# Optimization experiments

Hardware: AMD Instinct MI355X
Metric: run time of the kernel (lower is better)

## Reference

```python
import jax, jax.numpy as jnp
import numpy as np

MAX_DIST = 3          # census patch radius -> 7x7 neighborhood
PATCH = 2 * MAX_DIST + 1


def _warp(img, flow):
    """Bilinear warp (Resample2d): sample img at (x + u, y + v). Coords clamped to border."""
    B, C, H, W = img.shape
    gy, gx = jnp.meshgrid(jnp.arange(H, dtype=img.dtype), jnp.arange(W, dtype=img.dtype), indexing='ij')
    x = gx[None] + flow[:, 0]           # [B,H,W]
    y = gy[None] + flow[:, 1]
    x0 = jnp.floor(x); y0 = jnp.floor(y)
    wx = x - x0; wy = y - y0            # bilinear weights
    x0i = jnp.clip(x0, 0, W - 1).astype(jnp.int32)
    x1i = jnp.clip(x0 + 1.0, 0, W - 1).astype(jnp.int32)
    y0i = jnp.clip(y0, 0, H - 1).astype(jnp.int32)
    y1i = jnp.clip(y0 + 1.0, 0, H - 1).astype(jnp.int32)

    def gather(im_b, yi, xi):           # im_b [C,H,W], yi/xi [H,W] -> [C,H,W]
        return im_b[:, yi, xi]
    g = jax.vmap(gather)
    Ia = g(img, y0i, x0i); Ib = g(img, y0i, x1i)
    Ic = g(img, y1i, x0i); Id = g(img, y1i, x1i)
    wx = wx[:, None]; wy = wy[:, None]  # [B,1,H,W]
    return Ia * (1 - wx) * (1 - wy) + Ib * wx * (1 - wy) + Ic * (1 - wx) * wy + Id * wx * wy


def _census_transform(image):
    """Ternary census transform: grayscale, extract 7x7 patches, normalized center differences."""
    gray = (0.299 * image[:, 0:1] + 0.587 * image[:, 1:2] + 0.114 * image[:, 2:3]) * 255.0
    w = jnp.eye(PATCH * PATCH, dtype=image.dtype).reshape(PATCH * PATCH, 1, PATCH, PATCH)
    patches = jax.lax.conv_general_dilated(
        gray, w, window_strides=(1, 1), padding=[(MAX_DIST, MAX_DIST)] * 2,
        dimension_numbers=('NCHW', 'OIHW', 'NCHW'))   # [B,49,H,W]
    t = patches - gray
    return t / jnp.sqrt(0.81 + t * t)


def _border_mask(B, H, W, dtype):
    m = jnp.zeros((H, W), dtype).at[MAX_DIST:H - MAX_DIST, MAX_DIST:W - MAX_DIST].set(1.0)
    return jnp.broadcast_to(m[None, None], (B, 1, H, W))


def _charbonnier(x, mask, alpha=0.45, eps=0.001):
    err = (x * x + eps * eps) ** alpha * mask
    return jnp.sum(err) / x.size


def _census_loss(im1, im2_warped, mask):
    t1 = _census_transform(im1)
    t2 = _census_transform(im2_warped)
    d = (t1 - t2) ** 2
    dist = jnp.sum(d / (0.1 + d), axis=1, keepdims=True)   # soft Hamming distance [B,1,H,W]
    B, _, H, W = dist.shape
    return _charbonnier(dist, mask * _border_mask(B, H, W, dist.dtype))


def setup_inputs() -> dict:
    key = jax.random.key(0)
    ks = jax.random.split(key, 6)
    B, H, W = 4, 320, 768
    return {
        'former': jax.random.uniform(ks[0], (B, 3, H, W), jnp.float32),
        'latter': jax.random.uniform(ks[1], (B, 3, H, W), jnp.float32),
        'disp_est_scale': jax.random.normal(ks[2], (B, 2, H, W), jnp.float32) * 3.0,
        'disp_est_scale_2': jax.random.normal(ks[3], (B, 2, H, W), jnp.float32) * 3.0,
        'fw_mask': jax.random.uniform(ks[4], (B, 1, H, W), jnp.float32),
        'bw_mask': jax.random.uniform(ks[5], (B, 1, H, W), jnp.float32),
    }


def reference(former, latter, disp_est_scale, disp_est_scale_2, fw_mask, bw_mask):
    left_est = _warp(latter, disp_est_scale)
    image_loss = _census_loss(former, left_est, fw_mask)
    right_est = _warp(former, disp_est_scale_2)
    image_loss_2 = _census_loss(latter, right_est, bw_mask)
    return (image_loss, image_loss_2)
```

## Files before the change

kernel.cpp:

```cpp
#include <hip/hip_runtime.h>

#define BB 4
#define H 320
#define W 768
#define P (H*W)
#define NPIX (BB*P)

#define TX 32
#define TY 8
#define TW (TX+6)
#define TH (TY+6)
#define HALO (TW*TH)
#define NBX (W/TX)
#define NBY (H/TY)
#define NBLK (NBX*NBY*BB)

typedef float f4 __attribute__((ext_vector_type(4)));

__global__ void gray_kernel(const float* __restrict__ former,
                            const float* __restrict__ latter,
                            float* __restrict__ gf, float* __restrict__ gl) {
    int idx = blockIdx.x * blockDim.x + threadIdx.x;
    if (idx >= NPIX) return;
    int b = idx / P;
    int r = idx - b * P;
    const float* f = former + (size_t)b * 3 * P + r;
    const float* l = latter + (size_t)b * 3 * P + r;
    gf[idx] = (0.299f * f[0] + 0.587f * f[P] + 0.114f * f[2 * P]) * 255.f;
    gl[idx] = (0.299f * l[0] + 0.587f * l[P] + 0.114f * l[2 * P]) * 255.f;
}

__device__ __forceinline__ float bilinear(const float* __restrict__ img, float fx, float fy) {
    float x0 = floorf(fx), y0 = floorf(fy);
    float wx = fx - x0, wy = fy - y0;
    float x0c = fminf(fmaxf(x0,       0.f), (float)(W - 1));
    float x1c = fminf(fmaxf(x0 + 1.f, 0.f), (float)(W - 1));
    float y0c = fminf(fmaxf(y0,       0.f), (float)(H - 1));
    float y1c = fminf(fmaxf(y0 + 1.f, 0.f), (float)(H - 1));
    int x0i = (int)x0c, x1i = (int)x1c, y0i = (int)y0c, y1i = (int)y1c;
    float Ia = img[y0i * W + x0i], Ib = img[y0i * W + x1i];
    float Ic = img[y1i * W + x0i], Id = img[y1i * W + x1i];
    float omx = 1.f - wx, omy = 1.f - wy;
    return Ia * omx * omy + Ib * wx * omy + Ic * omx * wy + Id * wx * wy;
}

__global__ __launch_bounds__(256, 5)
void fused_kernel(const float* __restrict__ gf, const float* __restrict__ gl,
                  const float* __restrict__ flow1, const float* __restrict__ flow2,
                  const float* __restrict__ fw_mask, const float* __restrict__ bw_mask,
                  float* __restrict__ partials) {
    __shared__ f4 sT[HALO];
    const int b   = blockIdx.z;
    const int tx0 = blockIdx.x * TX;
    const int ty0 = blockIdx.y * TY;
    const int tid = threadIdx.x;

    const float* pGF = gf + (size_t)b * P;
    const float* pGL = gl + (size_t)b * P;
    const float* pF1 = flow1 + (size_t)b * 2 * P;
    const float* pF2 = flow2 + (size_t)b * 2 * P;

    for (int i = tid; i < HALO; i += 256) {
        int ly = i / TW, lx = i - ly * TW;
        int gx = min(max(tx0 - 3 + lx, 0), W - 1);
        int gy = min(max(ty0 - 3 + ly, 0), H - 1);
        int o = gy * W + gx;
        float A = pGF[o];
        float C = pGL[o];
        float u1 = pF1[o], v1 = pF1[P + o];
        float u2 = pF2[o], v2 = pF2[P + o];
        float Bv = bilinear(pGL, (float)gx + u1, (float)gy + v1);
        float D  = bilinear(pGF, (float)gx + u2, (float)gy + v2);
        sT[i] = (f4){A, Bv, C, D};
    }
    __syncthreads();

    const int lx = tid & 31, ly = tid >> 5;
    const int x = tx0 + lx, y = ty0 + ly;
    float sum1 = 0.f, sum2 = 0.f;

    if (x >= 3 && x < W - 3 && y >= 3 && y < H - 3) {
        const float m1 = fw_mask[(size_t)b * P + y * W + x];
        const float m2 = bw_mask[(size_t)b * P + y * W + x];
        const int c = (ly + 3) * TW + (lx + 3);
        const f4 cv = sT[c];
        const float c1 = cv.x, c2 = cv.y, c3 = cv.z, c4 = cv.w;
        float acc1a = 0.f, acc1b = 0.f, acc2a = 0.f, acc2b = 0.f;
#pragma unroll
        for (int dy = 0; dy < 7; ++dy) {
            const int ro = (ly + dy) * TW + lx;
#pragma unroll
            for (int dx = 0; dx < 7; ++dx) {
                if (dy == 3 && dx == 3) continue;
                const f4 n = sT[ro + dx];
                {
                    const float a  = n.x - c1;
                    const float bb = n.y - c2;
                    const float t1 = a  * __builtin_amdgcn_rsqf(fmaf(a,  a,  0.81f));
                    const float t2 = bb * __builtin_amdgcn_rsqf(fmaf(bb, bb, 0.81f));
                    float d = t1 - t2; d *= d;
                    const float r = __builtin_amdgcn_rcpf(d + 0.1f);
                    if (dx & 1) acc1a = fmaf(d, r, acc1a);
                    else        acc1b = fmaf(d, r, acc1b);
                }
                {
                    const float a  = n.z - c3;
                    const float bb = n.w - c4;
                    const float t1 = a  * __builtin_amdgcn_rsqf(fmaf(a,  a,  0.81f));
                    const float t2 = bb * __builtin_amdgcn_rsqf(fmaf(bb, bb, 0.81f));
                    float d = t1 - t2; d *= d;
                    const float r = __builtin_amdgcn_rcpf(d + 0.1f);
                    if (dx & 1) acc2a = fmaf(d, r, acc2a);
                    else        acc2b = fmaf(d, r, acc2b);
                }
            }
        }
        const float dist1 = acc1a + acc1b;
        const float dist2 = acc2a + acc2b;
        sum1 = exp2f(0.45f * log2f(fmaf(dist1, dist1, 1e-6f))) * m1;
        sum2 = exp2f(0.45f * log2f(fmaf(dist2, dist2, 1e-6f))) * m2;
    }

#pragma unroll
    for (int off = 32; off; off >>= 1) {
        sum1 += __shfl_down(sum1, off, 64);
        sum2 += __shfl_down(sum2, off, 64);
    }
    __shared__ float red[8];
    const int wave = tid >> 6, lane = tid & 63;
    if (lane == 0) { red[wave] = sum1; red[4 + wave] = sum2; }
    __syncthreads();
    if (tid == 0) {
        const int blk = (blockIdx.z * NBY + blockIdx.y) * NBX + blockIdx.x;
        partials[2 * blk]     = red[0] + red[1] + red[2] + red[3];
        partials[2 * blk + 1] = red[4] + red[5] + red[6] + red[7];
    }
}

__global__ __launch_bounds__(256)
void reduce_kernel(const float* __restrict__ partials, float* __restrict__ out) {
    const int tid = threadIdx.x;
    float s1 = 0.f, s2 = 0.f;
    for (int i = tid; i < NBLK; i += 256) {
        s1 += partials[2 * i];
        s2 += partials[2 * i + 1];
    }
#pragma unroll
    for (int off = 32; off; off >>= 1) {
        s1 += __shfl_down(s1, off, 64);
        s2 += __shfl_down(s2, off, 64);
    }
    __shared__ float red[8];
    const int wave = tid >> 6, lane = tid & 63;
    if (lane == 0) { red[wave] = s1; red[4 + wave] = s2; }
    __syncthreads();
    if (tid == 0) {
        out[0] = (red[0] + red[1] + red[2] + red[3]) * (1.0f / NPIX);
        out[1] = (red[4] + red[5] + red[6] + red[7]) * (1.0f / NPIX);
    }
}

extern "C" void kernel_launch(void* const* d_in, const int* in_sizes, int n_in,
                              void* d_out, int out_size, void* d_ws, size_t ws_size,
                              hipStream_t stream) {
    (void)in_sizes; (void)n_in; (void)out_size; (void)ws_size;
    const float* former  = (const float*)d_in[0];
    const float* latter  = (const float*)d_in[1];
    const float* flow1   = (const float*)d_in[2];
    const float* flow2   = (const float*)d_in[3];
    const float* fw_mask = (const float*)d_in[4];
    const float* bw_mask = (const float*)d_in[5];
    float* out = (float*)d_out;
    float* ws  = (float*)d_ws;
    float* gf       = ws;
    float* gl       = ws + NPIX;
    float* partials = ws + 2 * (size_t)NPIX;

    gray_kernel<<<(NPIX + 255) / 256, 256, 0, stream>>>(former, latter, gf, gl);
    fused_kernel<<<dim3(NBX, NBY, BB), 256, 0, stream>>>(gf, gl, flow1, flow2,
                                                         fw_mask, bw_mask, partials);
    reduce_kernel<<<1, 256, 0, stream>>>(partials, out);
}
```

Baseline: 136.2 us.

## Fuse grayscale conversion and final reduction into census kernel; merge per-neighbor divisions

Removes the separate grayscale pass and computes gray values on the fly from the 3-channel images, including inside the bilinear gathers. This costs 3x more gathered loads per bilinear sample. Replaces the standalone reduce kernel with a last-block-done atomic counter, which needs a memset launch to reset the counter. Rewrites the per-neighbor math so the two rsq calls become one on a product and the two reciprocals are shared across both losses, lowering transcendental count at some numerical risk.

```diff
diff --git a/kernel.cpp b/kernel.cpp
--- a/kernel.cpp
+++ b/kernel.cpp
@@ -17,20 +17,11 @@
 
 typedef float f4 __attribute__((ext_vector_type(4)));
 
-__global__ void gray_kernel(const float* __restrict__ former,
-                            const float* __restrict__ latter,
-                            float* __restrict__ gf, float* __restrict__ gl) {
-    int idx = blockIdx.x * blockDim.x + threadIdx.x;
-    if (idx >= NPIX) return;
-    int b = idx / P;
-    int r = idx - b * P;
-    const float* f = former + (size_t)b * 3 * P + r;
-    const float* l = latter + (size_t)b * 3 * P + r;
-    gf[idx] = (0.299f * f[0] + 0.587f * f[P] + 0.114f * f[2 * P]) * 255.f;
-    gl[idx] = (0.299f * l[0] + 0.587f * l[P] + 0.114f * l[2 * P]) * 255.f;
+__device__ __forceinline__ float gray_at(const float* __restrict__ img3, int o) {
+    return (0.299f * img3[o] + 0.587f * img3[P + o] + 0.114f * img3[2 * P + o]) * 255.f;
 }
 
-__device__ __forceinline__ float bilinear(const float* __restrict__ img, float fx, float fy) {
+__device__ __forceinline__ float bilinear_gray(const float* __restrict__ img3, float fx, float fy) {
     float x0 = floorf(fx), y0 = floorf(fy);
     float wx = fx - x0, wy = fy - y0;
     float x0c = fminf(fmaxf(x0,       0.f), (float)(W - 1));
@@ -38,39 +29,40 @@
     float y0c = fminf(fmaxf(y0,       0.f), (float)(H - 1));
     float y1c = fminf(fmaxf(y0 + 1.f, 0.f), (float)(H - 1));
     int x0i = (int)x0c, x1i = (int)x1c, y0i = (int)y0c, y1i = (int)y1c;
-    float Ia = img[y0i * W + x0i], Ib = img[y0i * W + x1i];
-    float Ic = img[y1i * W + x0i], Id = img[y1i * W + x1i];
+    float Ia = gray_at(img3, y0i * W + x0i), Ib = gray_at(img3, y0i * W + x1i);
+    float Ic = gray_at(img3, y1i * W + x0i), Id = gray_at(img3, y1i * W + x1i);
     float omx = 1.f - wx, omy = 1.f - wy;
     return Ia * omx * omy + Ib * wx * omy + Ic * omx * wy + Id * wx * wy;
 }
 
 __global__ __launch_bounds__(256, 5)
-void fused_kernel(const float* __restrict__ gf, const float* __restrict__ gl,
+void fused_kernel(const float* __restrict__ former, const float* __restrict__ latter,
                   const float* __restrict__ flow1, const float* __restrict__ flow2,
                   const float* __restrict__ fw_mask, const float* __restrict__ bw_mask,
-                  float* __restrict__ partials) {
+                  float* __restrict__ partials, unsigned* __restrict__ counter,
+                  float* __restrict__ out) {
     __shared__ f4 sT[HALO];
     const int b   = blockIdx.z;
     const int tx0 = blockIdx.x * TX;
     const int ty0 = blockIdx.y * TY;
     const int tid = threadIdx.x;
 
-    const float* pGF = gf + (size_t)b * P;
-    const float* pGL = gl + (size_t)b * P;
-    const float* pF1 = flow1 + (size_t)b * 2 * P;
-    const float* pF2 = flow2 + (size_t)b * 2 * P;
+    const float* pF3 = former + (size_t)b * 3 * P;
+    const float* pL3 = latter + (size_t)b * 3 * P;
+    const float* pU1 = flow1 + (size_t)b * 2 * P;
+    const float* pU2 = flow2 + (size_t)b * 2 * P;
 
     for (int i = tid; i < HALO; i += 256) {
         int ly = i / TW, lx = i - ly * TW;
         int gx = min(max(tx0 - 3 + lx, 0), W - 1);
         int gy = min(max(ty0 - 3 + ly, 0), H - 1);
         int o = gy * W + gx;
-        float A = pGF[o];
-        float C = pGL[o];
-        float u1 = pF1[o], v1 = pF1[P + o];
-        float u2 = pF2[o], v2 = pF2[P + o];
-        float Bv = bilinear(pGL, (float)gx + u1, (float)gy + v1);
-        float D  = bilinear(pGF, (float)gx + u2, (float)gy + v2);
+        float A = gray_at(pF3, o);
+        float C = gray_at(pL3, o);
+        float u1 = pU1[o], v1 = pU1[P + o];
+        float u2 = pU2[o], v2 = pU2[P + o];
+        float Bv = bilinear_gray(pL3, (float)gx + u1, (float)gy + v1);
+        float D  = bilinear_gray(pF3, (float)gx + u2, (float)gy + v2);
         sT[i] = (f4){A, Bv, C, D};
     }
     __syncthreads();
@@ -93,26 +85,24 @@
             for (int dx = 0; dx < 7; ++dx) {
                 if (dy == 3 && dx == 3) continue;
                 const f4 n = sT[ro + dx];
-                {
-                    const float a  = n.x - c1;
-                    const float bb = n.y - c2;
-                    const float t1 = a  * __builtin_amdgcn_rsqf(fmaf(a,  a,  0.81f));
-                    const float t2 = bb * __builtin_amdgcn_rsqf(fmaf(bb, bb, 0.81f));
-                    float d = t1 - t2; d *= d;
-                    const float r = __builtin_amdgcn_rcpf(d + 0.1f);
-                    if (dx & 1) acc1a = fmaf(d, r, acc1a);
-                    else        acc1b = fmaf(d, r, acc1b);
-                }
-                {
-                    const float a  = n.z - c3;
-                    const float bb = n.w - c4;
-                    const float t1 = a  * __builtin_amdgcn_rsqf(fmaf(a,  a,  0.81f));
-                    const float t2 = bb * __builtin_amdgcn_rsqf(fmaf(bb, bb, 0.81f));
-                    float d = t1 - t2; d *= d;
-                    const float r = __builtin_amdgcn_rcpf(d + 0.1f);
-                    if (dx & 1) acc2a = fmaf(d, r, acc2a);
-                    else        acc2b = fmaf(d, r, acc2b);
-                }
+                const float a1 = n.x - c1, b1 = n.y - c2;
+                const float qa1 = fmaf(a1, a1, 0.81f), qb1 = fmaf(b1, b1, 0.81f);
+                const float pr1 = qa1 * qb1;
+                const float s1 = __builtin_amdgcn_rsqf(pr1);
+                const float num1 = fmaf(-0.81f, qa1 + qb1, pr1 + pr1);
+                const float d1 = fmaf(num1, s1 * s1, ((a1 * b1) * s1) * -2.f);
+                const float a2 = n.z - c3, b2 = n.w - c4;
+                const float qa2 = fmaf(a2, a2, 0.81f), qb2 = fmaf(b2, b2, 0.81f);
+                const float pr2 = qa2 * qb2;
+                const float s2 = __builtin_amdgcn_rsqf(pr2);
+                const float num2 = fmaf(-0.81f, qa2 + qb2, pr2 + pr2);
+                const float d2 = fmaf(num2, s2 * s2, ((a2 * b2) * s2) * -2.f);
+                const float e1 = d1 + 0.1f, e2 = d2 + 0.1f;
+                const float ir = __builtin_amdgcn_rcpf(e1 * e2);
+                const float g1 = (d1 * e2) * ir;
+                const float g2 = (d2 * e1) * ir;
+                if (dx & 1) { acc1a += g1; acc2a += g2; }
+                else        { acc1b += g1; acc2b += g2; }
             }
         }
         const float dist1 = acc1a + acc1b;
@@ -135,28 +125,33 @@
         partials[2 * blk]     = red[0] + red[1] + red[2] + red[3];
         partials[2 * blk + 1] = red[4] + red[5] + red[6] + red[7];
     }
-}
 
-__global__ __launch_bounds__(256)
-void reduce_kernel(const float* __restrict__ partials, float* __restrict__ out) {
-    const int tid = threadIdx.x;
-    float s1 = 0.f, s2 = 0.f;
-    for (int i = tid; i < NBLK; i += 256) {
-        s1 += partials[2 * i];
-        s2 += partials[2 * i + 1];
+    __shared__ unsigned sLast;
+    if (tid == 0) {
+        __threadfence();
+        unsigned prev = __hip_atomic_fetch_add(counter, 1u, __ATOMIC_ACQ_REL,
+                                               __HIP_MEMORY_SCOPE_AGENT);
+        sLast = (prev == NBLK - 1) ? 1u : 0u;
     }
+    __syncthreads();
+    if (sLast) {
+        float s1 = 0.f, s2 = 0.f;
+        for (int i = tid; i < NBLK; i += 256) {
+            s1 += __hip_atomic_load(&partials[2 * i],     __ATOMIC_RELAXED, __HIP_MEMORY_SCOPE_AGENT);
+            s2 += __hip_atomic_load(&partials[2 * i + 1], __ATOMIC_RELAXED, __HIP_MEMORY_SCOPE_AGENT);
+        }
 #pragma unroll
-    for (int off = 32; off; off >>= 1) {
-        s1 += __shfl_down(s1, off, 64);
-        s2 += __shfl_down(s2, off, 64);
-    }
-    __shared__ float red[8];
-    const int wave = tid >> 6, lane = tid & 63;
-    if (lane == 0) { red[wave] = s1; red[4 + wave] = s2; }
-    __syncthreads();
-    if (tid == 0) {
-        out[0] = (red[0] + red[1] + red[2] + red[3]) * (1.0f / NPIX);
-        out[1] = (red[4] + red[5] + red[6] + red[7]) * (1.0f / NPIX);
+        for (int off = 32; off; off >>= 1) {
+            s1 += __shfl_down(s1, off, 64);
+            s2 += __shfl_down(s2, off, 64);
+        }
+        __shared__ float red2[8];
+        if (lane == 0) { red2[wave] = s1; red2[4 + wave] = s2; }
+        __syncthreads();
+        if (tid == 0) {
+            out[0] = (red2[0] + red2[1] + red2[2] + red2[3]) * (1.0f / NPIX);
+            out[1] = (red2[4] + red2[5] + red2[6] + red2[7]) * (1.0f / NPIX);
+        }
     }
 }
 
@@ -172,12 +167,11 @@
     const float* bw_mask = (const float*)d_in[5];
     float* out = (float*)d_out;
     float* ws  = (float*)d_ws;
-    float* gf       = ws;
-    float* gl       = ws + NPIX;
-    float* partials = ws + 2 * (size_t)NPIX;
+    float* partials   = ws;
+    unsigned* counter = (unsigned*)(ws + 2 * NBLK);
 
-    gray_kernel<<<(NPIX + 255) / 256, 256, 0, stream>>>(former, latter, gf, gl);
-    fused_kernel<<<dim3(NBX, NBY, BB), 256, 0, stream>>>(gf, gl, flow1, flow2,
-                                                         fw_mask, bw_mask, partials);
-    reduce_kernel<<<1, 256, 0, stream>>>(partials, out);
+    hipMemsetAsync(counter, 0, sizeof(unsigned), stream);
+    fused_kernel<<<dim3(NBX, NBY, BB), 256, 0, stream>>>(former, latter, flow1, flow2,
+                                                         fw_mask, bw_mask,
+                                                         partials, counter, out);
 }
```

Result: slower. 357.7 us (+162.7%).
